# Kernel optimization log

Measured on AMD Instinct MI355X. Metric: run time of the kernel, lower is better.

Reference implementation:

```python
import jax, jax.numpy as jnp
import numpy as np

N_NODES = 50000
N_EDGES = 800000
NEG_SLOPE = 0.2


def _edge_softmax(scores, dst, n):
    # scores: [E, H]; softmax over edges grouped by destination node
    m = jax.ops.segment_max(scores, dst, num_segments=n)          # [N, H]
    ex = jnp.exp(scores - m[dst])                                 # [E, H]
    s = jax.ops.segment_sum(ex, dst, num_segments=n)              # [N, H]
    return ex / s[dst]


def _gat_layer(h, W, attn_l, attn_r, bias, src, dst, n, heads, out_d):
    feat = (h @ W).reshape(n, heads, out_d)                       # [N, H, D]
    el = jnp.sum(feat * attn_l, axis=-1)                          # [N, H]
    er = jnp.sum(feat * attn_r, axis=-1)                          # [N, H]
    e = jax.nn.leaky_relu(el[src] + er[dst], NEG_SLOPE)           # [E, H]
    alpha = _edge_softmax(e, dst, n)                              # [E, H]
    msg = feat[src] * alpha[:, :, None]                           # [E, H, D]
    rst = jax.ops.segment_sum(msg, dst, num_segments=n)           # [N, H, D]
    return rst + bias.reshape(1, heads, out_d)


def setup_inputs() -> dict:
    key = jax.random.key(0)
    ks = jax.random.split(key, 12)
    in_dim, hid, heads, out_dim = 128, 64, 4, 64
    sc = 0.1
    return {
        "emb": jax.random.normal(ks[0], (N_NODES, in_dim), jnp.float32),
        "src": jax.random.randint(ks[1], (N_EDGES,), 0, N_NODES, jnp.int32),
        "dst": jax.random.randint(ks[2], (N_EDGES,), 0, N_NODES, jnp.int32),
        "W1": jax.random.normal(ks[3], (in_dim, heads * hid), jnp.float32) * sc,
        "attn_l1": jax.random.normal(ks[4], (1, heads, hid), jnp.float32) * sc,
        "attn_r1": jax.random.normal(ks[5], (1, heads, hid), jnp.float32) * sc,
        "b1": jax.random.normal(ks[6], (heads * hid,), jnp.float32) * sc,
        "W2": jax.random.normal(ks[7], (heads * hid, out_dim), jnp.float32) * sc,
        "attn_l2": jax.random.normal(ks[8], (1, 1, out_dim), jnp.float32) * sc,
        "attn_r2": jax.random.normal(ks[9], (1, 1, out_dim), jnp.float32) * sc,
        "b2": jax.random.normal(ks[10], (out_dim,), jnp.float32) * sc,
    }


def reference(emb, src, dst, W1, attn_l1, attn_r1, b1, W2, attn_l2, attn_r2, b2):
    n = emb.shape[0]
    h = _gat_layer(emb, W1, attn_l1, attn_r1, b1, src, dst, n, 4, 64)   # [N,4,64]
    h = jax.nn.relu(h).reshape(n, 4 * 64)                                # [N,256]
    h = _gat_layer(h, W2, attn_l2, attn_r2, b2, src, dst, n, 1, 64)      # [N,1,64]
    return h.reshape(n, 64)
```

## Files before the change

kernel.cpp:

```cpp
#include <hip/hip_runtime.h>
#include <hip/hip_bf16.h>
#include <math.h>

#define DIV_UP(a,b) (((a)+(b)-1)/(b))

typedef __attribute__((ext_vector_type(8))) short short8v;
typedef __attribute__((ext_vector_type(4))) float f32x4;

__device__ __forceinline__ float bf_lo(unsigned u){ union{unsigned x; float f;} v; v.x = u << 16; return v.f; }
__device__ __forceinline__ float bf_hi(unsigned u){ union{unsigned x; float f;} v; v.x = u & 0xffff0000u; return v.f; }
__device__ __forceinline__ unsigned short f2bf(float f){
  union{float f; unsigned u;} v; v.f = f;
  unsigned r = v.u + 0x7fff + ((v.u >> 16) & 1);
  return (unsigned short)(r >> 16);
}
__device__ __forceinline__ unsigned packbf(float a, float b){
  return (unsigned)f2bf(a) | ((unsigned)f2bf(b) << 16);
}
__device__ __forceinline__ float lrelu(float x){ return x > 0.f ? x : 0.2f*x; }

__global__ void k_count_deg(const int* __restrict__ dst, int* __restrict__ deg, int E){
  int i = blockIdx.x*blockDim.x + threadIdx.x;
  if (i < E) atomicAdd(&deg[dst[i]], 1);
}

__global__ __launch_bounds__(256) void k_scan1(const int* __restrict__ deg,
                                               int* __restrict__ blocksum, int N){
  int b = blockIdx.x;
  int base = b*1024 + threadIdx.x*4;
  int s = 0;
  if (base + 3 < N){
    int4 v = *(const int4*)&deg[base];
    s = v.x + v.y + v.z + v.w;
  } else {
    for (int i = 0; i < 4; i++){ int idx = base + i; if (idx < N) s += deg[idx]; }
  }
  #pragma unroll
  for (int o = 32; o; o >>= 1) s += __shfl_down(s, o);
  __shared__ int ws[4];
  int wid = threadIdx.x >> 6, lane = threadIdx.x & 63;
  if (lane == 0) ws[wid] = s;
  __syncthreads();
  if (threadIdx.x == 0) blocksum[b] = ws[0] + ws[1] + ws[2] + ws[3];
}

__global__ void k_scan2(int* __restrict__ blocksum, int nb){
  int lane = threadIdx.x;
  int carry = 0;
  for (int base = 0; base < nb; base += 64){
    int idx = base + lane;
    int orig = (idx < nb) ? blocksum[idx] : 0;
    int v = orig;
    #pragma unroll
    for (int o = 1; o < 64; o <<= 1){ int t = __shfl_up(v, o); if (lane >= o) v += t; }
    if (idx < nb) blocksum[idx] = carry + v - orig;
    carry += __shfl(v, 63);
  }
}

__global__ __launch_bounds__(256) void k_scan3(const int* __restrict__ deg,
                                               const int* __restrict__ blockoff,
                                               int* __restrict__ row_start,
                                               int* __restrict__ cursor, int N){
  int b = blockIdx.x;
  int base = b*1024 + threadIdx.x*4;
  int v[4];
  #pragma unroll
  for (int i = 0; i < 4; i++){ int idx = base + i; v[i] = (idx < N) ? deg[idx] : 0; }
  int s = v[0] + v[1] + v[2] + v[3];
  int lane = threadIdx.x & 63, wid = threadIdx.x >> 6;
  int inc = s;
  #pragma unroll
  for (int o = 1; o < 64; o <<= 1){ int t = __shfl_up(inc, o); if (lane >= o) inc += t; }
  __shared__ int wsum[4];
  if (lane == 63) wsum[wid] = inc;
  __syncthreads();
  int woff = 0;
  #pragma unroll
  for (int i = 0; i < 4; i++) if (i < wid) woff += wsum[i];
  int run = blockoff[b] + woff + inc - s;
  #pragma unroll
  for (int i = 0; i < 4; i++){
    int idx = base + i;
    if (idx < N){ row_start[idx] = run; cursor[idx] = run; run += v[i]; }
  }
  if (base < N && base + 4 >= N) row_start[N] = run;
}

__global__ void k_fillw4(const int* __restrict__ dst, const int* __restrict__ src,
                         int* __restrict__ cursor, int* __restrict__ srcp,
                         int* __restrict__ dstp,
                         const float4* __restrict__ el4, const float4* __restrict__ er4,
                         float4* __restrict__ w4, int E){
  int i = blockIdx.x*blockDim.x + threadIdx.x;
  if (i < E){
    int d = dst[i], s = src[i];
    int p = atomicAdd(&cursor[d], 1);
    srcp[p] = s; dstp[p] = d;
    float4 l = el4[s], r = er4[d];
    float4 w;
    w.x = __expf(lrelu(l.x + r.x));
    w.y = __expf(lrelu(l.y + r.y));
    w.z = __expf(lrelu(l.z + r.z));
    w.w = __expf(lrelu(l.w + r.w));
    w4[p] = w;
  }
}

__global__ void k_edgew1(const int* __restrict__ srcp, const int* __restrict__ dstp,
                         const float* __restrict__ el, const float* __restrict__ er,
                         float* __restrict__ w1, int E){
  int i = blockIdx.x*blockDim.x + threadIdx.x;
  if (i < E) w1[i] = __expf(lrelu(el[srcp[i]] + er[dstp[i]]));
}

template<int K, int H, bool ABF>
__global__ __launch_bounds__(256) void k_gemm_mfma(const void* __restrict__ Av,
      const float* __restrict__ B, int ldb,
      unsigned short* __restrict__ Cbf,
      const float* __restrict__ al, const float* __restrict__ ar,
      float* __restrict__ el, float* __restrict__ er, int M){
  constexpr int KP = K + 8;
  __shared__ alignas(16) __hip_bfloat16 At[64][KP];
  __shared__ alignas(16) __hip_bfloat16 Bt[64][KP];
  __shared__ float elp[2][64], erp[2][64];
  const int tid = threadIdx.x;
  const int lane = tid & 63, w = tid >> 6;
  const int mw = w >> 1, nw = w & 1;
  const int m0 = blockIdx.x * 64, by = blockIdx.y, n0 = by * 64;

  if constexpr (!ABF){
    const float* A = (const float*)Av;
    #pragma unroll
    for (int i = 0; i < K/16; i++){
      int q = tid + i*256;
      int row = q / (K/4), c4 = q % (K/4);
      float4 a = make_float4(0.f,0.f,0.f,0.f);
      if (m0 + row < M) a = *(const float4*)&A[(size_t)(m0+row)*K + c4*4];
      *(uint2*)&At[row][c4*4] = make_uint2(packbf(a.x,a.y), packbf(a.z,a.w));
    }
  } else {
    const __hip_bfloat16* A = (const __hip_bfloat16*)Av;
    #pragma unroll
    for (int i = 0; i < K/32; i++){
      int q = tid + i*256;
      int row = q / (K/8), c8 = q % (K/8);
      uint4 u = make_uint4(0,0,0,0);
      if (m0 + row < M) u = *(const uint4*)&A[(size_t)(m0+row)*K + c8*8];
      *(uint4*)&At[row][c8*8] = u;
    }
  }
  #pragma unroll
  for (int i = 0; i < K/16; i++){
    int q = tid + i*256;
    int c = q & 63, k4 = q >> 6;
    float b0 = B[(size_t)(k4*4+0)*ldb + n0 + c];
    float b1 = B[(size_t)(k4*4+1)*ldb + n0 + c];
    float b2 = B[(size_t)(k4*4+2)*ldb + n0 + c];
    float b3 = B[(size_t)(k4*4+3)*ldb + n0 + c];
    *(uint2*)&Bt[c][k4*4] = make_uint2(packbf(b0,b1), packbf(b2,b3));
  }
  __syncthreads();

  f32x4 acc[2][2];
  #pragma unroll
  for (int i = 0; i < 2; i++)
    #pragma unroll
    for (int j = 0; j < 2; j++)
      #pragma unroll
      for (int r = 0; r < 4; r++) acc[i][j][r] = 0.f;

  const int rbase = mw*32, cbase = nw*32;
  const int fr = lane & 15, fg = lane >> 4;
  #pragma unroll
  for (int ks = 0; ks < K/32; ks++){
    short8v a0 = *(const short8v*)&At[rbase + fr     ][ks*32 + fg*8];
    short8v a1 = *(const short8v*)&At[rbase + 16 + fr][ks*32 + fg*8];
    short8v b0 = *(const short8v*)&Bt[cbase + fr     ][ks*32 + fg*8];
    short8v b1 = *(const short8v*)&Bt[cbase + 16 + fr][ks*32 + fg*8];
    acc[0][0] = __builtin_amdgcn_mfma_f32_16x16x32_bf16(a0, b0, acc[0][0], 0,0,0);
    acc[0][1] = __builtin_amdgcn_mfma_f32_16x16x32_bf16(a0, b1, acc[0][1], 0,0,0);
    acc[1][0] = __builtin_amdgcn_mfma_f32_16x16x32_bf16(a1, b0, acc[1][0], 0,0,0);
    acc[1][1] = __builtin_amdgcn_mfma_f32_16x16x32_bf16(a1, b1, acc[1][1], 0,0,0);
  }

  float alv[2], arv[2];
  #pragma unroll
  for (int nt = 0; nt < 2; nt++){
    int col = cbase + nt*16 + fr;
    alv[nt] = al[by*64 + col];
    arv[nt] = ar[by*64 + col];
  }
  #pragma unroll
  for (int mt = 0; mt < 2; mt++){
    #pragma unroll
    for (int r = 0; r < 4; r++){
      float pl = acc[mt][0][r]*alv[0] + acc[mt][1][r]*alv[1];
      float pr = acc[mt][0][r]*arv[0] + acc[mt][1][r]*arv[1];
      #pragma unroll
      for (int o = 1; o < 16; o <<= 1){ pl += __shfl_xor(pl, o); pr += __shfl_xor(pr, o); }
      if (fr == 0){
        int rl = rbase + mt*16 + fg*4 + r;
        elp[nw][rl] = pl; erp[nw][rl] = pr;
      }
    }
  }
  const int NN = H*64;
  #pragma unroll
  for (int mt = 0; mt < 2; mt++){
    #pragma unroll
    for (int r = 0; r < 4; r++){
      int row = m0 + rbase + mt*16 + fg*4 + r;
      if (row < M){
        #pragma unroll
        for (int nt = 0; nt < 2; nt++)
          Cbf[(size_t)row*NN + n0 + cbase + nt*16 + fr] = f2bf(acc[mt][nt][r]);
      }
    }
  }
  __syncthreads();
  if (tid < 64){
    int row = m0 + tid;
    if (row < M){
      el[(size_t)row*H + by] = elp[0][tid] + elp[1][tid];
      er[(size_t)row*H + by] = erp[0][tid] + erp[1][tid];
    }
  }
}

__global__ __launch_bounds__(256) void k_gath4(const char* __restrict__ featb,
      const float* __restrict__ w4, const int* __restrict__ row_start,
      const int* __restrict__ srcp, const float* __restrict__ bias,
      __hip_bfloat16* __restrict__ outb, int N, int nwaves){
  int wv = threadIdx.x >> 6, lane = threadIdx.x & 63;
  int g = lane >> 4, j = lane & 15, h = j >> 2;
  const char* fb = featb + (unsigned)(j << 5);

  int n = blockIdx.x*4 + wv;
  if (n >= N) return;
  int rs = row_start[n], re = row_start[n+1];

  while (true){
    int deg = re - rs;
    int nn = n + nwaves;
    int rs_n = 0, re_n = 0;
    if (nn < N){ rs_n = row_start[nn]; re_n = row_start[nn+1]; }

    float acc[16];
    #pragma unroll
    for (int k = 0; k < 16; k++) acc[k] = 0.f;
    float Sacc = 0.f;

    int i = 0;
    int full = deg & ~15;
    for (; i < full; i += 16){
      float wb[4]; uint4 u0[4], u1[4];
      #pragma unroll
      for (int k = 0; k < 4; k++){
        int e = rs + i + k*4 + g;
        int sb = srcp[e];
        wb[k] = w4[(size_t)e*4 + h];
        const char* p = fb + (size_t)sb*512u;
        u0[k] = *(const uint4*)p;
        u1[k] = *(const uint4*)(p + 16);
      }
      #pragma unroll
      for (int k = 0; k < 4; k++){
        float wk = wb[k];
        Sacc += wk;
        acc[0]  += bf_lo(u0[k].x)*wk; acc[1]  += bf_hi(u0[k].x)*wk;
        acc[2]  += bf_lo(u0[k].y)*wk; acc[3]  += bf_hi(u0[k].y)*wk;
        acc[4]  += bf_lo(u0[k].z)*wk; acc[5]  += bf_hi(u0[k].z)*wk;
        acc[6]  += bf_lo(u0[k].w)*wk; acc[7]  += bf_hi(u0[k].w)*wk;
        acc[8]  += bf_lo(u1[k].x)*wk; acc[9]  += bf_hi(u1[k].x)*wk;
        acc[10] += bf_lo(u1[k].y)*wk; acc[11] += bf_hi(u1[k].y)*wk;
        acc[12] += bf_lo(u1[k].z)*wk; acc[13] += bf_hi(u1[k].z)*wk;
        acc[14] += bf_lo(u1[k].w)*wk; acc[15] += bf_hi(u1[k].w)*wk;
      }
    }
    if (i < deg){
      float wb[4]; uint4 u0[4], u1[4];
      #pragma unroll
      for (int k = 0; k < 4; k++){
        int e = i + k*4 + g;
        wb[k] = 0.f;
        u0[k] = make_uint4(0,0,0,0); u1[k] = make_uint4(0,0,0,0);
        if (e < deg){
          int sb = srcp[rs + e];
          wb[k] = w4[(size_t)(rs + e)*4 + h];
          const char* p = fb + (size_t)sb*512u;
          u0[k] = *(const uint4*)p;
          u1[k] = *(const uint4*)(p + 16);
        }
      }
      #pragma unroll
      for (int k = 0; k < 4; k++){
        float wk = wb[k];
        Sacc += wk;
        acc[0]  += bf_lo(u0[k].x)*wk; acc[1]  += bf_hi(u0[k].x)*wk;
        acc[2]  += bf_lo(u0[k].y)*wk; acc[3]  += bf_hi(u0[k].y)*wk;
        acc[4]  += bf_lo(u0[k].z)*wk; acc[5]  += bf_hi(u0[k].z)*wk;
        acc[6]  += bf_lo(u0[k].w)*wk; acc[7]  += bf_hi(u0[k].w)*wk;
        acc[8]  += bf_lo(u1[k].x)*wk; acc[9]  += bf_hi(u1[k].x)*wk;
        acc[10] += bf_lo(u1[k].y)*wk; acc[11] += bf_hi(u1[k].y)*wk;
        acc[12] += bf_lo(u1[k].z)*wk; acc[13] += bf_hi(u1[k].z)*wk;
        acc[14] += bf_lo(u1[k].w)*wk; acc[15] += bf_hi(u1[k].w)*wk;
      }
    }

    #pragma unroll
    for (int k = 0; k < 16; k++){
      acc[k] += __shfl_xor(acc[k], 16);
      acc[k] += __shfl_xor(acc[k], 32);
    }
    Sacc += __shfl_xor(Sacc, 16);
    Sacc += __shfl_xor(Sacc, 32);
    if (g == 0){
      float inv = (deg > 0 && Sacc > 0.f) ? 1.f / Sacc : 0.f;
      float4 b0 = *(const float4*)&bias[j*16 + 0];
      float4 b1 = *(const float4*)&bias[j*16 + 4];
      float4 b2 = *(const float4*)&bias[j*16 + 8];
      float4 b3 = *(const float4*)&bias[j*16 + 12];
      float v[16];
      v[0]=acc[0]*inv+b0.x;  v[1]=acc[1]*inv+b0.y;  v[2]=acc[2]*inv+b0.z;  v[3]=acc[3]*inv+b0.w;
      v[4]=acc[4]*inv+b1.x;  v[5]=acc[5]*inv+b1.y;  v[6]=acc[6]*inv+b1.z;  v[7]=acc[7]*inv+b1.w;
      v[8]=acc[8]*inv+b2.x;  v[9]=acc[9]*inv+b2.y;  v[10]=acc[10]*inv+b2.z; v[11]=acc[11]*inv+b2.w;
      v[12]=acc[12]*inv+b3.x; v[13]=acc[13]*inv+b3.y; v[14]=acc[14]*inv+b3.z; v[15]=acc[15]*inv+b3.w;
      #pragma unroll
      for (int k = 0; k < 16; k++) v[k] = fmaxf(v[k], 0.f);
      uint4 o0, o1;
      o0.x = packbf(v[0], v[1]);   o0.y = packbf(v[2], v[3]);
      o0.z = packbf(v[4], v[5]);   o0.w = packbf(v[6], v[7]);
      o1.x = packbf(v[8], v[9]);   o1.y = packbf(v[10], v[11]);
      o1.z = packbf(v[12], v[13]); o1.w = packbf(v[14], v[15]);
      uint4* op = (uint4*)outb + (size_t)n*32 + (j << 1);
      op[0] = o0; op[1] = o1;
    }

    if (nn >= N) break;
    n = nn; rs = rs_n; re = re_n;
  }
}

__global__ __launch_bounds__(256) void k_gath1(const char* __restrict__ featb,
      const float* __restrict__ w1, const int* __restrict__ row_start,
      const int* __restrict__ srcp, const float* __restrict__ bias,
      float* __restrict__ out, int N, int nwaves){
  int wv = threadIdx.x >> 6, lane = threadIdx.x & 63;
  int g = lane >> 4, j = lane & 15;
  const char* fb = featb + (unsigned)(j << 3);

  int n = blockIdx.x*4 + wv;
  if (n >= N) return;
  int rs = row_start[n], re = row_start[n+1];

  while (true){
    int deg = re - rs;
    int nn = n + nwaves;
    int rs_n = 0, re_n = 0;
    if (nn < N){ rs_n = row_start[nn]; re_n = row_start[nn+1]; }

    float acc[4] = {0.f, 0.f, 0.f, 0.f};
    float Sacc = 0.f;

    int i = 0;
    int full = deg & ~15;
    for (; i < full; i += 16){
      float wb[4]; uint2 u[4];
      #pragma unroll
      for (int k = 0; k < 4; k++){
        int e = rs + i + k*4 + g;
        int sb = srcp[e];
        wb[k] = w1[e];
        u[k] = *(const uint2*)(fb + (size_t)sb*128u);
      }
      #pragma unroll
      for (int k = 0; k < 4; k++){
        float wk = wb[k];
        Sacc += wk;
        acc[0] += bf_lo(u[k].x)*wk; acc[1] += bf_hi(u[k].x)*wk;
        acc[2] += bf_lo(u[k].y)*wk; acc[3] += bf_hi(u[k].y)*wk;
      }
    }
    if (i < deg){
      float wb[4]; uint2 u[4];
      #pragma unroll
      for (int k = 0; k < 4; k++){
        int e = i + k*4 + g;
        wb[k] = 0.f;
        u[k] = make_uint2(0,0);
        if (e < deg){
          int sb = srcp[rs + e];
          wb[k] = w1[rs + e];
          u[k] = *(const uint2*)(fb + (size_t)sb*128u);
        }
      }
      #pragma unroll
      for (int k = 0; k < 4; k++){
        float wk = wb[k];
        Sacc += wk;
        acc[0] += bf_lo(u[k].x)*wk; acc[1] += bf_hi(u[k].x)*wk;
        acc[2] += bf_lo(u[k].y)*wk; acc[3] += bf_hi(u[k].y)*wk;
      }
    }

    #pragma unroll
    for (int k = 0; k < 4; k++){
      acc[k] += __shfl_xor(acc[k], 16);
      acc[k] += __shfl_xor(acc[k], 32);
    }
    Sacc += __shfl_xor(Sacc, 16);
    Sacc += __shfl_xor(Sacc, 32);
    if (g == 0){
      float inv = (deg > 0 && Sacc > 0.f) ? 1.f / Sacc : 0.f;
      float4 b = *(const float4*)&bias[j*4];
      float4 o;
      o.x = acc[0]*inv + b.x; o.y = acc[1]*inv + b.y;
      o.z = acc[2]*inv + b.z; o.w = acc[3]*inv + b.w;
      *(float4*)&out[(size_t)n*64 + j*4] = o;
    }

    if (nn >= N) break;
    n = nn; rs = rs_n; re = re_n;
  }
}

extern "C" void kernel_launch(void* const* d_in, const int* in_sizes, int n_in,
                              void* d_out, int out_size, void* d_ws, size_t ws_size,
                              hipStream_t stream) {
  const float* emb = (const float*)d_in[0];
  const int*   src = (const int*)d_in[1];
  const int*   dst = (const int*)d_in[2];
  const float* W1  = (const float*)d_in[3];
  const float* al1 = (const float*)d_in[4];
  const float* ar1 = (const float*)d_in[5];
  const float* b1  = (const float*)d_in[6];
  const float* W2  = (const float*)d_in[7];
  const float* al2 = (const float*)d_in[8];
  const float* ar2 = (const float*)d_in[9];
  const float* b2  = (const float*)d_in[10];
  float* out = (float*)d_out;

  const int N = in_sizes[0] / 128;
  const int E = in_sizes[1];

  char* p = (char*)d_ws;
  auto alloc = [&](size_t bytes) -> void* {
    void* r = (void*)p; p += (bytes + 255) & ~(size_t)255; return r;
  };
  __hip_bfloat16* feat1b = (__hip_bfloat16*)alloc((size_t)N*256*2);
  __hip_bfloat16* h1b    = (__hip_bfloat16*)alloc((size_t)N*256*2);
  __hip_bfloat16* feat2b = (__hip_bfloat16*)alloc((size_t)N*64*2);
  float* el1             = (float*)alloc((size_t)N*4*4);
  float* er1             = (float*)alloc((size_t)N*4*4);
  float* el2             = (float*)alloc((size_t)N*4);
  float* er2             = (float*)alloc((size_t)N*4);
  int*   deg             = (int*)alloc((size_t)N*4);
  int*   row_start       = (int*)alloc((size_t)(N+1)*4);
  int*   cursor          = (int*)alloc((size_t)N*4);
  int*   blocksum        = (int*)alloc((size_t)DIV_UP(N,1024)*4);
  int*   srcp            = (int*)alloc((size_t)E*4);
  int*   dstp            = (int*)alloc((size_t)E*4);
  float* w4              = (float*)alloc((size_t)E*16);
  float* w1              = w4;

  const int nb = DIV_UP(N, 1024);
  const int gblocks = min(DIV_UP(N, 4), 2048);
  const int nwaves  = gblocks * 4;

  hipMemsetAsync(deg, 0, (size_t)N*4, stream);
  k_count_deg<<<DIV_UP(E,256), 256, 0, stream>>>(dst, deg, E);
  k_scan1<<<nb, 256, 0, stream>>>(deg, blocksum, N);
  k_scan2<<<1, 64, 0, stream>>>(blocksum, nb);
  k_scan3<<<nb, 256, 0, stream>>>(deg, blocksum, row_start, cursor, N);

  k_gemm_mfma<128,4,false><<<dim3(DIV_UP(N,64), 4), 256, 0, stream>>>(
      emb, W1, 256, (unsigned short*)feat1b, al1, ar1, el1, er1, N);
  k_fillw4<<<DIV_UP(E,256), 256, 0, stream>>>(dst, src, cursor, srcp, dstp,
      (const float4*)el1, (const float4*)er1, (float4*)w4, E);
  k_gath4<<<gblocks, 256, 0, stream>>>((const char*)feat1b, w4, row_start,
                                       srcp, b1, h1b, N, nwaves);
  k_gemm_mfma<256,1,true><<<dim3(DIV_UP(N,64), 1), 256, 0, stream>>>(
      h1b, W2, 64, (unsigned short*)feat2b, al2, ar2, el2, er2, N);
  k_edgew1<<<DIV_UP(E,256), 256, 0, stream>>>(srcp, dstp, el2, er2, w1, E);
  k_gath1<<<gblocks, 256, 0, stream>>>((const char*)feat2b, w1, row_start,
                                       srcp, b2, out, N, nwaves);
}
```

Measured before the change: 237.7 us.

## Aggregate raw embeddings before the layer-1 projection, then apply W1 per head

Layer 1 now gathers bf16 input embeddings (128-wide) along edges and applies W1 afterwards, instead of gathering projected 256-wide features. Attention logits are computed directly from the embeddings using precomputed W1·attn vectors. The cost this targets is per-edge gather traffic: each edge now reads 256 B instead of 512 B. In exchange, each node stores a 4-head aggregate (512 bf16 values, larger than before) that the new per-head GEMM must re-read, and the gather does four times the FMAs per loaded element.

Result: slower. 264.0 us (+11.0%).

```diff
diff --git a/kernel.cpp b/kernel.cpp
--- a/kernel.cpp
+++ b/kernel.cpp
@@ -85,6 +85,46 @@
     if (idx < N){ row_start[idx] = run; cursor[idx] = run; run += v[i]; }
   }
   if (base < N && base + 4 >= N) row_start[N] = run;
+}
+
+__global__ __launch_bounds__(256) void k_prepvec(const float* __restrict__ W1,
+      const float* __restrict__ al, const float* __restrict__ ar,
+      float* __restrict__ W1al4, float* __restrict__ W1ar4){
+  int t = blockIdx.x*256 + threadIdx.x;
+  if (t >= 1024) return;
+  int k = t >> 3, idx = t & 7, h = idx >> 1, side = idx & 1;
+  const float* v = (side ? ar : al) + h*64;
+  const float* wrow = W1 + (size_t)k*256 + h*64;
+  float s = 0.f;
+  #pragma unroll 8
+  for (int d = 0; d < 64; d++) s += wrow[d]*v[d];
+  (side ? W1ar4 : W1al4)[k*4 + h] = s;
+}
+
+__global__ __launch_bounds__(256) void k_embcast(const float2* __restrict__ emb2,
+      const float4* __restrict__ W1al4, const float4* __restrict__ W1ar4,
+      unsigned* __restrict__ embb, float4* __restrict__ el4, float4* __restrict__ er4,
+      int N){
+  int wv = threadIdx.x >> 6, lane = threadIdx.x & 63;
+  int n = blockIdx.x*4 + wv;
+  if (n >= N) return;
+  float2 a = emb2[(size_t)n*64 + lane];
+  embb[(size_t)n*64 + lane] = packbf(a.x, a.y);
+  float4 wl0 = W1al4[2*lane], wl1 = W1al4[2*lane+1];
+  float4 wr0 = W1ar4[2*lane], wr1 = W1ar4[2*lane+1];
+  float4 pl, pr;
+  pl.x = a.x*wl0.x + a.y*wl1.x; pl.y = a.x*wl0.y + a.y*wl1.y;
+  pl.z = a.x*wl0.z + a.y*wl1.z; pl.w = a.x*wl0.w + a.y*wl1.w;
+  pr.x = a.x*wr0.x + a.y*wr1.x; pr.y = a.x*wr0.y + a.y*wr1.y;
+  pr.z = a.x*wr0.z + a.y*wr1.z; pr.w = a.x*wr0.w + a.y*wr1.w;
+  #pragma unroll
+  for (int o = 1; o < 64; o <<= 1){
+    pl.x += __shfl_xor(pl.x, o); pl.y += __shfl_xor(pl.y, o);
+    pl.z += __shfl_xor(pl.z, o); pl.w += __shfl_xor(pl.w, o);
+    pr.x += __shfl_xor(pr.x, o); pr.y += __shfl_xor(pr.y, o);
+    pr.z += __shfl_xor(pr.z, o); pr.w += __shfl_xor(pr.w, o);
+  }
+  if (lane == 0){ el4[n] = pl; er4[n] = pr; }
 }
 
 __global__ void k_fillw4(const int* __restrict__ dst, const int* __restrict__ src,
@@ -114,6 +154,186 @@
   if (i < E) w1[i] = __expf(lrelu(el[srcp[i]] + er[dstp[i]]));
 }
 
+__global__ __launch_bounds__(256) void k_gath4e(const char* __restrict__ embb,
+      const float4* __restrict__ w4, const int* __restrict__ row_start,
+      const int* __restrict__ srcp, uint4* __restrict__ aggb, int N, int nwaves){
+  int wv = threadIdx.x >> 6, lane = threadIdx.x & 63;
+  int g = lane >> 4, j = lane & 15;
+  const char* fb = embb + (unsigned)(j << 4);
+
+  int n = blockIdx.x*4 + wv;
+  if (n >= N) return;
+  int rs = row_start[n], re = row_start[n+1];
+
+  while (true){
+    int deg = re - rs;
+    int nn = n + nwaves;
+    int rs_n = 0, re_n = 0;
+    if (nn < N){ rs_n = row_start[nn]; re_n = row_start[nn+1]; }
+
+    float acc[4][8];
+    #pragma unroll
+    for (int h = 0; h < 4; h++)
+      #pragma unroll
+      for (int d = 0; d < 8; d++) acc[h][d] = 0.f;
+    float S0 = 0.f, S1 = 0.f, S2 = 0.f, S3 = 0.f;
+
+    int i = 0;
+    int full = deg & ~15;
+    for (; i < full; i += 16){
+      uint4 u[4]; float4 w[4];
+      #pragma unroll
+      for (int k = 0; k < 4; k++){
+        int e = rs + i + k*4 + g;
+        int sb = srcp[e];
+        w[k] = w4[e];
+        u[k] = *(const uint4*)(fb + (size_t)sb*256u);
+      }
+      #pragma unroll
+      for (int k = 0; k < 4; k++){
+        float4 wk = w[k];
+        S0 += wk.x; S1 += wk.y; S2 += wk.z; S3 += wk.w;
+        float x[8];
+        x[0]=bf_lo(u[k].x); x[1]=bf_hi(u[k].x); x[2]=bf_lo(u[k].y); x[3]=bf_hi(u[k].y);
+        x[4]=bf_lo(u[k].z); x[5]=bf_hi(u[k].z); x[6]=bf_lo(u[k].w); x[7]=bf_hi(u[k].w);
+        #pragma unroll
+        for (int d = 0; d < 8; d++){
+          acc[0][d] += x[d]*wk.x; acc[1][d] += x[d]*wk.y;
+          acc[2][d] += x[d]*wk.z; acc[3][d] += x[d]*wk.w;
+        }
+      }
+    }
+    if (i < deg){
+      uint4 u[4]; float4 w[4];
+      #pragma unroll
+      for (int k = 0; k < 4; k++){
+        int e = i + k*4 + g;
+        w[k] = make_float4(0.f,0.f,0.f,0.f);
+        u[k] = make_uint4(0,0,0,0);
+        if (e < deg){
+          int sb = srcp[rs + e];
+          w[k] = w4[rs + e];
+          u[k] = *(const uint4*)(fb + (size_t)sb*256u);
+        }
+      }
+      #pragma unroll
+      for (int k = 0; k < 4; k++){
+        float4 wk = w[k];
+        S0 += wk.x; S1 += wk.y; S2 += wk.z; S3 += wk.w;
+        float x[8];
+        x[0]=bf_lo(u[k].x); x[1]=bf_hi(u[k].x); x[2]=bf_lo(u[k].y); x[3]=bf_hi(u[k].y);
+        x[4]=bf_lo(u[k].z); x[5]=bf_hi(u[k].z); x[6]=bf_lo(u[k].w); x[7]=bf_hi(u[k].w);
+        #pragma unroll
+        for (int d = 0; d < 8; d++){
+          acc[0][d] += x[d]*wk.x; acc[1][d] += x[d]*wk.y;
+          acc[2][d] += x[d]*wk.z; acc[3][d] += x[d]*wk.w;
+        }
+      }
+    }
+
+    #pragma unroll
+    for (int h = 0; h < 4; h++)
+      #pragma unroll
+      for (int d = 0; d < 8; d++){
+        acc[h][d] += __shfl_xor(acc[h][d], 16);
+        acc[h][d] += __shfl_xor(acc[h][d], 32);
+      }
+    S0 += __shfl_xor(S0, 16); S0 += __shfl_xor(S0, 32);
+    S1 += __shfl_xor(S1, 16); S1 += __shfl_xor(S1, 32);
+    S2 += __shfl_xor(S2, 16); S2 += __shfl_xor(S2, 32);
+    S3 += __shfl_xor(S3, 16); S3 += __shfl_xor(S3, 32);
+
+    if (g == 0){
+      float Sv[4] = {S0, S1, S2, S3};
+      #pragma unroll
+      for (int h = 0; h < 4; h++){
+        float inv = (deg > 0 && Sv[h] > 0.f) ? 1.f/Sv[h] : 0.f;
+        uint4 o;
+        o.x = packbf(acc[h][0]*inv, acc[h][1]*inv);
+        o.y = packbf(acc[h][2]*inv, acc[h][3]*inv);
+        o.z = packbf(acc[h][4]*inv, acc[h][5]*inv);
+        o.w = packbf(acc[h][6]*inv, acc[h][7]*inv);
+        aggb[(size_t)n*64 + h*16 + j] = o;
+      }
+    }
+
+    if (nn >= N) break;
+    n = nn; rs = rs_n; re = re_n;
+  }
+}
+
+__global__ __launch_bounds__(256) void k_gemm_agg(const __hip_bfloat16* __restrict__ A,
+      const float* __restrict__ B,
+      const float* __restrict__ bias,
+      unsigned short* __restrict__ C,
+      int M){
+  __shared__ alignas(16) __hip_bfloat16 At[64][136];
+  __shared__ alignas(16) __hip_bfloat16 Bt[64][136];
+  const int tid = threadIdx.x;
+  const int lane = tid & 63, w = tid >> 6;
+  const int mw = w >> 1, nw = w & 1;
+  const int m0 = blockIdx.x * 64, by = blockIdx.y, n0 = by * 64;
+
+  #pragma unroll
+  for (int i = 0; i < 4; i++){
+    int q = tid + i*256;
+    int row = q >> 4, c8 = q & 15;
+    uint4 u = make_uint4(0,0,0,0);
+    if (m0 + row < M) u = *(const uint4*)&A[(size_t)(m0+row)*512 + by*128 + c8*8];
+    *(uint4*)&At[row][c8*8] = u;
+  }
+  #pragma unroll
+  for (int i = 0; i < 8; i++){
+    int q = tid + i*256;
+    int c = q & 63, k4 = q >> 6;
+    float b0 = B[(size_t)(k4*4+0)*256 + n0 + c];
+    float b1 = B[(size_t)(k4*4+1)*256 + n0 + c];
+    float b2 = B[(size_t)(k4*4+2)*256 + n0 + c];
+    float b3 = B[(size_t)(k4*4+3)*256 + n0 + c];
+    *(uint2*)&Bt[c][k4*4] = make_uint2(packbf(b0,b1), packbf(b2,b3));
+  }
+  __syncthreads();
+
+  f32x4 acc[2][2];
+  #pragma unroll
+  for (int i = 0; i < 2; i++)
+    #pragma unroll
+    for (int jj = 0; jj < 2; jj++)
+      #pragma unroll
+      for (int r = 0; r < 4; r++) acc[i][jj][r] = 0.f;
+
+  const int rbase = mw*32, cbase = nw*32;
+  const int fr = lane & 15, fg = lane >> 4;
+  #pragma unroll
+  for (int ks = 0; ks < 4; ks++){
+    short8v a0 = *(const short8v*)&At[rbase + fr     ][ks*32 + fg*8];
+    short8v a1 = *(const short8v*)&At[rbase + 16 + fr][ks*32 + fg*8];
+    short8v b0 = *(const short8v*)&Bt[cbase + fr     ][ks*32 + fg*8];
+    short8v b1 = *(const short8v*)&Bt[cbase + 16 + fr][ks*32 + fg*8];
+    acc[0][0] = __builtin_amdgcn_mfma_f32_16x16x32_bf16(a0, b0, acc[0][0], 0,0,0);
+    acc[0][1] = __builtin_amdgcn_mfma_f32_16x16x32_bf16(a0, b1, acc[0][1], 0,0,0);
+    acc[1][0] = __builtin_amdgcn_mfma_f32_16x16x32_bf16(a1, b0, acc[1][0], 0,0,0);
+    acc[1][1] = __builtin_amdgcn_mfma_f32_16x16x32_bf16(a1, b1, acc[1][1], 0,0,0);
+  }
+
+  #pragma unroll
+  for (int mt = 0; mt < 2; mt++){
+    #pragma unroll
+    for (int r = 0; r < 4; r++){
+      int row = m0 + rbase + mt*16 + fg*4 + r;
+      if (row < M){
+        #pragma unroll
+        for (int nt = 0; nt < 2; nt++){
+          int col = cbase + nt*16 + fr;
+          float v = acc[mt][nt][r] + bias[n0 + col];
+          v = fmaxf(v, 0.f);
+          C[(size_t)row*256 + n0 + col] = f2bf(v);
+        }
+      }
+    }
+  }
+}
+
 template<int K, int H, bool ABF>
 __global__ __launch_bounds__(256) void k_gemm_mfma(const void* __restrict__ Av,
       const float* __restrict__ B, int ldb,
@@ -225,120 +445,6 @@
       el[(size_t)row*H + by] = elp[0][tid] + elp[1][tid];
       er[(size_t)row*H + by] = erp[0][tid] + erp[1][tid];
     }
-  }
-}
-
-__global__ __launch_bounds__(256) void k_gath4(const char* __restrict__ featb,
-      const float* __restrict__ w4, const int* __restrict__ row_start,
-      const int* __restrict__ srcp, const float* __restrict__ bias,
-      __hip_bfloat16* __restrict__ outb, int N, int nwaves){
-  int wv = threadIdx.x >> 6, lane = threadIdx.x & 63;
-  int g = lane >> 4, j = lane & 15, h = j >> 2;
-  const char* fb = featb + (unsigned)(j << 5);
-
-  int n = blockIdx.x*4 + wv;
-  if (n >= N) return;
-  int rs = row_start[n], re = row_start[n+1];
-
-  while (true){
-    int deg = re - rs;
-    int nn = n + nwaves;
-    int rs_n = 0, re_n = 0;
-    if (nn < N){ rs_n = row_start[nn]; re_n = row_start[nn+1]; }
-
-    float acc[16];
-    #pragma unroll
-    for (int k = 0; k < 16; k++) acc[k] = 0.f;
-    float Sacc = 0.f;
-
-    int i = 0;
-    int full = deg & ~15;
-    for (; i < full; i += 16){
-      float wb[4]; uint4 u0[4], u1[4];
-      #pragma unroll
-      for (int k = 0; k < 4; k++){
-        int e = rs + i + k*4 + g;
-        int sb = srcp[e];
-        wb[k] = w4[(size_t)e*4 + h];
-        const char* p = fb + (size_t)sb*512u;
-        u0[k] = *(const uint4*)p;
-        u1[k] = *(const uint4*)(p + 16);
-      }
-      #pragma unroll
-      for (int k = 0; k < 4; k++){
-        float wk = wb[k];
-        Sacc += wk;
-        acc[0]  += bf_lo(u0[k].x)*wk; acc[1]  += bf_hi(u0[k].x)*wk;
-        acc[2]  += bf_lo(u0[k].y)*wk; acc[3]  += bf_hi(u0[k].y)*wk;
-        acc[4]  += bf_lo(u0[k].z)*wk; acc[5]  += bf_hi(u0[k].z)*wk;
-        acc[6]  += bf_lo(u0[k].w)*wk; acc[7]  += bf_hi(u0[k].w)*wk;
-        acc[8]  += bf_lo(u1[k].x)*wk; acc[9]  += bf_hi(u1[k].x)*wk;
-        acc[10] += bf_lo(u1[k].y)*wk; acc[11] += bf_hi(u1[k].y)*wk;
-        acc[12] += bf_lo(u1[k].z)*wk; acc[13] += bf_hi(u1[k].z)*wk;
-        acc[14] += bf_lo(u1[k].w)*wk; acc[15] += bf_hi(u1[k].w)*wk;
-      }
-    }
-    if (i < deg){
-      float wb[4]; uint4 u0[4], u1[4];
-      #pragma unroll
-      for (int k = 0; k < 4; k++){
-        int e = i + k*4 + g;
-        wb[k] = 0.f;
-        u0[k] = make_uint4(0,0,0,0); u1[k] = make_uint4(0,0,0,0);
-        if (e < deg){
-          int sb = srcp[rs + e];
-          wb[k] = w4[(size_t)(rs + e)*4 + h];
-          const char* p = fb + (size_t)sb*512u;
-          u0[k] = *(const uint4*)p;
-          u1[k] = *(const uint4*)(p + 16);
-        }
-      }
-      #pragma unroll
-      for (int k = 0; k < 4; k++){
-        float wk = wb[k];
-        Sacc += wk;
-        acc[0]  += bf_lo(u0[k].x)*wk; acc[1]  += bf_hi(u0[k].x)*wk;
-        acc[2]  += bf_lo(u0[k].y)*wk; acc[3]  += bf_hi(u0[k].y)*wk;
-        acc[4]  += bf_lo(u0[k].z)*wk; acc[5]  += bf_hi(u0[k].z)*wk;
-        acc[6]  += bf_lo(u0[k].w)*wk; acc[7]  += bf_hi(u0[k].w)*wk;
-        acc[8]  += bf_lo(u1[k].x)*wk; acc[9]  += bf_hi(u1[k].x)*wk;
-        acc[10] += bf_lo(u1[k].y)*wk; acc[11] += bf_hi(u1[k].y)*wk;
-        acc[12] += bf_lo(u1[k].z)*wk; acc[13] += bf_hi(u1[k].z)*wk;
-        acc[14] += bf_lo(u1[k].w)*wk; acc[15] += bf_hi(u1[k].w)*wk;
-      }
-    }
-
-    #pragma unroll
-    for (int k = 0; k < 16; k++){
-      acc[k] += __shfl_xor(acc[k], 16);
-      acc[k] += __shfl_xor(acc[k], 32);
-    }
-    Sacc += __shfl_xor(Sacc, 16);
-    Sacc += __shfl_xor(Sacc, 32);
-    if (g == 0){
-      float inv = (deg > 0 && Sacc > 0.f) ? 1.f / Sacc : 0.f;
-      float4 b0 = *(const float4*)&bias[j*16 + 0];
-      float4 b1 = *(const float4*)&bias[j*16 + 4];
-      float4 b2 = *(const float4*)&bias[j*16 + 8];
-      float4 b3 = *(const float4*)&bias[j*16 + 12];
-      float v[16];
-      v[0]=acc[0]*inv+b0.x;  v[1]=acc[1]*inv+b0.y;  v[2]=acc[2]*inv+b0.z;  v[3]=acc[3]*inv+b0.w;
-      v[4]=acc[4]*inv+b1.x;  v[5]=acc[5]*inv+b1.y;  v[6]=acc[6]*inv+b1.z;  v[7]=acc[7]*inv+b1.w;
-      v[8]=acc[8]*inv+b2.x;  v[9]=acc[9]*inv+b2.y;  v[10]=acc[10]*inv+b2.z; v[11]=acc[11]*inv+b2.w;
-      v[12]=acc[12]*inv+b3.x; v[13]=acc[13]*inv+b3.y; v[14]=acc[14]*inv+b3.z; v[15]=acc[15]*inv+b3.w;
-      #pragma unroll
-      for (int k = 0; k < 16; k++) v[k] = fmaxf(v[k], 0.f);
-      uint4 o0, o1;
-      o0.x = packbf(v[0], v[1]);   o0.y = packbf(v[2], v[3]);
-      o0.z = packbf(v[4], v[5]);   o0.w = packbf(v[6], v[7]);
-      o1.x = packbf(v[8], v[9]);   o1.y = packbf(v[10], v[11]);
-      o1.z = packbf(v[12], v[13]); o1.w = packbf(v[14], v[15]);
-      uint4* op = (uint4*)outb + (size_t)n*32 + (j << 1);
-      op[0] = o0; op[1] = o1;
-    }
-
-    if (nn >= N) break;
-    n = nn; rs = rs_n; re = re_n;
   }
 }
 
@@ -448,9 +554,12 @@
   auto alloc = [&](size_t bytes) -> void* {
     void* r = (void*)p; p += (bytes + 255) & ~(size_t)255; return r;
   };
-  __hip_bfloat16* feat1b = (__hip_bfloat16*)alloc((size_t)N*256*2);
+  __hip_bfloat16* embb   = (__hip_bfloat16*)alloc((size_t)N*128*2);
+  __hip_bfloat16* aggb   = (__hip_bfloat16*)alloc((size_t)N*512*2);
   __hip_bfloat16* h1b    = (__hip_bfloat16*)alloc((size_t)N*256*2);
   __hip_bfloat16* feat2b = (__hip_bfloat16*)alloc((size_t)N*64*2);
+  float* W1al4           = (float*)alloc(128*4*4);
+  float* W1ar4           = (float*)alloc(128*4*4);
   float* el1             = (float*)alloc((size_t)N*4*4);
   float* er1             = (float*)alloc((size_t)N*4*4);
   float* el2             = (float*)alloc((size_t)N*4);
@@ -474,12 +583,17 @@
   k_scan2<<<1, 64, 0, stream>>>(blocksum, nb);
   k_scan3<<<nb, 256, 0, stream>>>(deg, blocksum, row_start, cursor, N);
 
-  k_gemm_mfma<128,4,false><<<dim3(DIV_UP(N,64), 4), 256, 0, stream>>>(
-      emb, W1, 256, (unsigned short*)feat1b, al1, ar1, el1, er1, N);
+  k_prepvec<<<4, 256, 0, stream>>>(W1, al1, ar1, W1al4, W1ar4);
+  k_embcast<<<DIV_UP(N,4), 256, 0, stream>>>((const float2*)emb,
+      (const float4*)W1al4, (const float4*)W1ar4,
+      (unsigned*)embb, (float4*)el1, (float4*)er1, N);
   k_fillw4<<<DIV_UP(E,256), 256, 0, stream>>>(dst, src, cursor, srcp, dstp,
       (const float4*)el1, (const float4*)er1, (float4*)w4, E);
-  k_gath4<<<gblocks, 256, 0, stream>>>((const char*)feat1b, w4, row_start,
-                                       srcp, b1, h1b, N, nwaves);
+  k_gath4e<<<gblocks, 256, 0, stream>>>((const char*)embb, (const float4*)w4,
+      row_start, srcp, (uint4*)aggb, N, nwaves);
+  k_gemm_agg<<<dim3(DIV_UP(N,64), 4), 256, 0, stream>>>(aggb, W1, b1,
+      (unsigned short*)h1b, N);
+
   k_gemm_mfma<256,1,true><<<dim3(DIV_UP(N,64), 1), 256, 0, stream>>>(
       h1b, W2, 64, (unsigned short*)feat2b, al2, ar2, el2, er2, N);
   k_edgew1<<<DIV_UP(E,256), 256, 0, stream>>>(srcp, dstp, el2, er2, w1, E);
```

## Fuse edge weight computation into gather kernels and widen layer-1 GEMM tile

Applied to the files above, without the earlier changes.

Edge attention weights (exp of leaky-relu of el[src]+er[dst]) are now computed inside the aggregation kernels instead of being materialised per edge by the fill and edgew1 kernels. This drops the w4/w1/dstp arrays and one kernel launch, which removes the per-edge weight writes and reads. The cost is an extra gather of el per edge inside the aggregation loop, plus recomputing exp per head lane. The layer-1 GEMM is replaced by a 512-thread kernel that covers all 256 output columns per block, so the A tile is loaded once per block instead of once per head.

Measured after the change: 261.7 us. 1.1x slower.

```diff
diff --git a/kernel.cpp b/kernel.cpp
--- a/kernel.cpp
+++ b/kernel.cpp
@@ -87,31 +87,112 @@
   if (base < N && base + 4 >= N) row_start[N] = run;
 }
 
-__global__ void k_fillw4(const int* __restrict__ dst, const int* __restrict__ src,
-                         int* __restrict__ cursor, int* __restrict__ srcp,
-                         int* __restrict__ dstp,
-                         const float4* __restrict__ el4, const float4* __restrict__ er4,
-                         float4* __restrict__ w4, int E){
+__global__ void k_fill(const int* __restrict__ dst, const int* __restrict__ src,
+                       int* __restrict__ cursor, int* __restrict__ srcp, int E){
   int i = blockIdx.x*blockDim.x + threadIdx.x;
-  if (i < E){
-    int d = dst[i], s = src[i];
-    int p = atomicAdd(&cursor[d], 1);
-    srcp[p] = s; dstp[p] = d;
-    float4 l = el4[s], r = er4[d];
-    float4 w;
-    w.x = __expf(lrelu(l.x + r.x));
-    w.y = __expf(lrelu(l.y + r.y));
-    w.z = __expf(lrelu(l.z + r.z));
-    w.w = __expf(lrelu(l.w + r.w));
-    w4[p] = w;
-  }
-}
-
-__global__ void k_edgew1(const int* __restrict__ srcp, const int* __restrict__ dstp,
-                         const float* __restrict__ el, const float* __restrict__ er,
-                         float* __restrict__ w1, int E){
-  int i = blockIdx.x*blockDim.x + threadIdx.x;
-  if (i < E) w1[i] = __expf(lrelu(el[srcp[i]] + er[dstp[i]]));
+  if (i < E){ int p = atomicAdd(&cursor[dst[i]], 1); srcp[p] = src[i]; }
+}
+
+__global__ __launch_bounds__(512) void k_gemm1h4(const float* __restrict__ A,
+      const float* __restrict__ B,
+      unsigned short* __restrict__ Cbf,
+      const float* __restrict__ al, const float* __restrict__ ar,
+      float* __restrict__ el, float* __restrict__ er, int M){
+  __shared__ alignas(16) __hip_bfloat16 At[64][136];
+  __shared__ alignas(16) __hip_bfloat16 Bt[256][136];
+  __shared__ float elp[8][64], erp[8][64];
+  const int tid = threadIdx.x;
+  const int lane = tid & 63, w = tid >> 6;
+  const int m0 = blockIdx.x * 64;
+  const int fr = lane & 15, fg = lane >> 4;
+  const int cbase = w * 32;
+
+  #pragma unroll
+  for (int i = 0; i < 4; i++){
+    int q = tid + i*512;
+    int row = q >> 5, c4 = q & 31;
+    float4 a = make_float4(0.f,0.f,0.f,0.f);
+    if (m0 + row < M) a = *(const float4*)&A[(size_t)(m0+row)*128 + c4*4];
+    *(uint2*)&At[row][c4*4] = make_uint2(packbf(a.x,a.y), packbf(a.z,a.w));
+  }
+  #pragma unroll
+  for (int i = 0; i < 16; i++){
+    int q = tid + i*512;
+    int col = q & 255, k4 = q >> 8;
+    float b0 = B[(size_t)(k4*4+0)*256 + col];
+    float b1 = B[(size_t)(k4*4+1)*256 + col];
+    float b2 = B[(size_t)(k4*4+2)*256 + col];
+    float b3 = B[(size_t)(k4*4+3)*256 + col];
+    *(uint2*)&Bt[col][k4*4] = make_uint2(packbf(b0,b1), packbf(b2,b3));
+  }
+  __syncthreads();
+
+  f32x4 acc[4][2];
+  #pragma unroll
+  for (int mt = 0; mt < 4; mt++)
+    #pragma unroll
+    for (int nt = 0; nt < 2; nt++)
+      #pragma unroll
+      for (int r = 0; r < 4; r++) acc[mt][nt][r] = 0.f;
+
+  #pragma unroll
+  for (int ks = 0; ks < 4; ks++){
+    short8v a0 = *(const short8v*)&At[ 0 + fr][ks*32 + fg*8];
+    short8v a1 = *(const short8v*)&At[16 + fr][ks*32 + fg*8];
+    short8v a2 = *(const short8v*)&At[32 + fr][ks*32 + fg*8];
+    short8v a3 = *(const short8v*)&At[48 + fr][ks*32 + fg*8];
+    short8v b0 = *(const short8v*)&Bt[cbase      + fr][ks*32 + fg*8];
+    short8v b1 = *(const short8v*)&Bt[cbase + 16 + fr][ks*32 + fg*8];
+    acc[0][0] = __builtin_amdgcn_mfma_f32_16x16x32_bf16(a0, b0, acc[0][0], 0,0,0);
+    acc[0][1] = __builtin_amdgcn_mfma_f32_16x16x32_bf16(a0, b1, acc[0][1], 0,0,0);
+    acc[1][0] = __builtin_amdgcn_mfma_f32_16x16x32_bf16(a1, b0, acc[1][0], 0,0,0);
+    acc[1][1] = __builtin_amdgcn_mfma_f32_16x16x32_bf16(a1, b1, acc[1][1], 0,0,0);
+    acc[2][0] = __builtin_amdgcn_mfma_f32_16x16x32_bf16(a2, b0, acc[2][0], 0,0,0);
+    acc[2][1] = __builtin_amdgcn_mfma_f32_16x16x32_bf16(a2, b1, acc[2][1], 0,0,0);
+    acc[3][0] = __builtin_amdgcn_mfma_f32_16x16x32_bf16(a3, b0, acc[3][0], 0,0,0);
+    acc[3][1] = __builtin_amdgcn_mfma_f32_16x16x32_bf16(a3, b1, acc[3][1], 0,0,0);
+  }
+
+  float alv[2], arv[2];
+  #pragma unroll
+  for (int nt = 0; nt < 2; nt++){
+    int col = cbase + nt*16 + fr;
+    alv[nt] = al[col]; arv[nt] = ar[col];
+  }
+  #pragma unroll
+  for (int mt = 0; mt < 4; mt++){
+    #pragma unroll
+    for (int r = 0; r < 4; r++){
+      float pl = acc[mt][0][r]*alv[0] + acc[mt][1][r]*alv[1];
+      float pr = acc[mt][0][r]*arv[0] + acc[mt][1][r]*arv[1];
+      #pragma unroll
+      for (int o = 1; o < 16; o <<= 1){ pl += __shfl_xor(pl, o); pr += __shfl_xor(pr, o); }
+      if (fr == 0){
+        int rl = mt*16 + fg*4 + r;
+        elp[w][rl] = pl; erp[w][rl] = pr;
+      }
+    }
+  }
+  #pragma unroll
+  for (int mt = 0; mt < 4; mt++){
+    #pragma unroll
+    for (int r = 0; r < 4; r++){
+      int row = m0 + mt*16 + fg*4 + r;
+      if (row < M){
+        #pragma unroll
+        for (int nt = 0; nt < 2; nt++)
+          Cbf[(size_t)row*256 + cbase + nt*16 + fr] = f2bf(acc[mt][nt][r]);
+      }
+    }
+  }
+  __syncthreads();
+  if (tid < 256){
+    int row = tid & 63, h = tid >> 6;
+    if (m0 + row < M){
+      el[(size_t)(m0+row)*4 + h] = elp[2*h][row] + elp[2*h+1][row];
+      er[(size_t)(m0+row)*4 + h] = erp[2*h][row] + erp[2*h+1][row];
+    }
+  }
 }
 
 template<int K, int H, bool ABF>
@@ -228,10 +309,11 @@
   }
 }
 
-__global__ __launch_bounds__(256) void k_gath4(const char* __restrict__ featb,
-      const float* __restrict__ w4, const int* __restrict__ row_start,
-      const int* __restrict__ srcp, const float* __restrict__ bias,
-      __hip_bfloat16* __restrict__ outb, int N, int nwaves){
+__global__ __launch_bounds__(256) void k_gath4w(const char* __restrict__ featb,
+      const float4* __restrict__ el4, const float4* __restrict__ er4,
+      const int* __restrict__ row_start, const int* __restrict__ srcp,
+      const float* __restrict__ bias, __hip_bfloat16* __restrict__ outb,
+      int N, int nwaves){
   int wv = threadIdx.x >> 6, lane = threadIdx.x & 63;
   int g = lane >> 4, j = lane & 15, h = j >> 2;
   const char* fb = featb + (unsigned)(j << 5);
@@ -246,6 +328,9 @@
     int rs_n = 0, re_n = 0;
     if (nn < N){ rs_n = row_start[nn]; re_n = row_start[nn+1]; }
 
+    float4 ern = er4[n];
+    float ernh = (h==0) ? ern.x : (h==1) ? ern.y : (h==2) ? ern.z : ern.w;
+
     float acc[16];
     #pragma unroll
     for (int k = 0; k < 16; k++) acc[k] = 0.f;
@@ -254,40 +339,46 @@
     int i = 0;
     int full = deg & ~15;
     for (; i < full; i += 16){
-      float wb[4]; uint4 u0[4], u1[4];
+      float wk[4]; uint4 u0[4], u1[4];
       #pragma unroll
       for (int k = 0; k < 4; k++){
         int e = rs + i + k*4 + g;
         int sb = srcp[e];
-        wb[k] = w4[(size_t)e*4 + h];
+        float4 elv = el4[sb];
+        float xh = (h==0) ? elv.x : (h==1) ? elv.y : (h==2) ? elv.z : elv.w;
+        xh += ernh; xh = xh > 0.f ? xh : 0.2f*xh;
+        wk[k] = __expf(xh);
         const char* p = fb + (size_t)sb*512u;
         u0[k] = *(const uint4*)p;
         u1[k] = *(const uint4*)(p + 16);
       }
       #pragma unroll
       for (int k = 0; k < 4; k++){
-        float wk = wb[k];
-        Sacc += wk;
-        acc[0]  += bf_lo(u0[k].x)*wk; acc[1]  += bf_hi(u0[k].x)*wk;
-        acc[2]  += bf_lo(u0[k].y)*wk; acc[3]  += bf_hi(u0[k].y)*wk;
-        acc[4]  += bf_lo(u0[k].z)*wk; acc[5]  += bf_hi(u0[k].z)*wk;
-        acc[6]  += bf_lo(u0[k].w)*wk; acc[7]  += bf_hi(u0[k].w)*wk;
-        acc[8]  += bf_lo(u1[k].x)*wk; acc[9]  += bf_hi(u1[k].x)*wk;
-        acc[10] += bf_lo(u1[k].y)*wk; acc[11] += bf_hi(u1[k].y)*wk;
-        acc[12] += bf_lo(u1[k].z)*wk; acc[13] += bf_hi(u1[k].z)*wk;
-        acc[14] += bf_lo(u1[k].w)*wk; acc[15] += bf_hi(u1[k].w)*wk;
+        float w = wk[k];
+        Sacc += w;
+        acc[0]  += bf_lo(u0[k].x)*w; acc[1]  += bf_hi(u0[k].x)*w;
+        acc[2]  += bf_lo(u0[k].y)*w; acc[3]  += bf_hi(u0[k].y)*w;
+        acc[4]  += bf_lo(u0[k].z)*w; acc[5]  += bf_hi(u0[k].z)*w;
+        acc[6]  += bf_lo(u0[k].w)*w; acc[7]  += bf_hi(u0[k].w)*w;
+        acc[8]  += bf_lo(u1[k].x)*w; acc[9]  += bf_hi(u1[k].x)*w;
+        acc[10] += bf_lo(u1[k].y)*w; acc[11] += bf_hi(u1[k].y)*w;
+        acc[12] += bf_lo(u1[k].z)*w; acc[13] += bf_hi(u1[k].z)*w;
+        acc[14] += bf_lo(u1[k].w)*w; acc[15] += bf_hi(u1[k].w)*w;
       }
     }
     if (i < deg){
-      float wb[4]; uint4 u0[4], u1[4];
+      float wk[4]; uint4 u0[4], u1[4];
       #pragma unroll
       for (int k = 0; k < 4; k++){
         int e = i + k*4 + g;
-        wb[k] = 0.f;
+        wk[k] = 0.f;
         u0[k] = make_uint4(0,0,0,0); u1[k] = make_uint4(0,0,0,0);
         if (e < deg){
           int sb = srcp[rs + e];
-          wb[k] = w4[(size_t)(rs + e)*4 + h];
+          float4 elv = el4[sb];
+          float xh = (h==0) ? elv.x : (h==1) ? elv.y : (h==2) ? elv.z : elv.w;
+          xh += ernh; xh = xh > 0.f ? xh : 0.2f*xh;
+          wk[k] = __expf(xh);
           const char* p = fb + (size_t)sb*512u;
           u0[k] = *(const uint4*)p;
           u1[k] = *(const uint4*)(p + 16);
@@ -295,16 +386,16 @@
       }
       #pragma unroll
       for (int k = 0; k < 4; k++){
-        float wk = wb[k];
-        Sacc += wk;
-        acc[0]  += bf_lo(u0[k].x)*wk; acc[1]  += bf_hi(u0[k].x)*wk;
-        acc[2]  += bf_lo(u0[k].y)*wk; acc[3]  += bf_hi(u0[k].y)*wk;
-        acc[4]  += bf_lo(u0[k].z)*wk; acc[5]  += bf_hi(u0[k].z)*wk;
-        acc[6]  += bf_lo(u0[k].w)*wk; acc[7]  += bf_hi(u0[k].w)*wk;
-        acc[8]  += bf_lo(u1[k].x)*wk; acc[9]  += bf_hi(u1[k].x)*wk;
-        acc[10] += bf_lo(u1[k].y)*wk; acc[11] += bf_hi(u1[k].y)*wk;
-        acc[12] += bf_lo(u1[k].z)*wk; acc[13] += bf_hi(u1[k].z)*wk;
-        acc[14] += bf_lo(u1[k].w)*wk; acc[15] += bf_hi(u1[k].w)*wk;
+        float w = wk[k];
+        Sacc += w;
+        acc[0]  += bf_lo(u0[k].x)*w; acc[1]  += bf_hi(u0[k].x)*w;
+        acc[2]  += bf_lo(u0[k].y)*w; acc[3]  += bf_hi(u0[k].y)*w;
+        acc[4]  += bf_lo(u0[k].z)*w; acc[5]  += bf_hi(u0[k].z)*w;
+        acc[6]  += bf_lo(u0[k].w)*w; acc[7]  += bf_hi(u0[k].w)*w;
+        acc[8]  += bf_lo(u1[k].x)*w; acc[9]  += bf_hi(u1[k].x)*w;
+        acc[10] += bf_lo(u1[k].y)*w; acc[11] += bf_hi(u1[k].y)*w;
+        acc[12] += bf_lo(u1[k].z)*w; acc[13] += bf_hi(u1[k].z)*w;
+        acc[14] += bf_lo(u1[k].w)*w; acc[15] += bf_hi(u1[k].w)*w;
       }
     }
 
@@ -342,10 +433,10 @@
   }
 }
 
-__global__ __launch_bounds__(256) void k_gath1(const char* __restrict__ featb,
-      const float* __restrict__ w1, const int* __restrict__ row_start,
-      const int* __restrict__ srcp, const float* __restrict__ bias,
-      float* __restrict__ out, int N, int nwaves){
+__global__ __launch_bounds__(256) void k_gath1w(const char* __restrict__ featb,
+      const float* __restrict__ el, const float* __restrict__ er,
+      const int* __restrict__ row_start, const int* __restrict__ srcp,
+      const float* __restrict__ bias, float* __restrict__ out, int N, int nwaves){
   int wv = threadIdx.x >> 6, lane = threadIdx.x & 63;
   int g = lane >> 4, j = lane & 15;
   const char* fb = featb + (unsigned)(j << 3);
@@ -360,47 +451,52 @@
     int rs_n = 0, re_n = 0;
     if (nn < N){ rs_n = row_start[nn]; re_n = row_start[nn+1]; }
 
+    float ern = er[n];
     float acc[4] = {0.f, 0.f, 0.f, 0.f};
     float Sacc = 0.f;
 
     int i = 0;
     int full = deg & ~15;
     for (; i < full; i += 16){
-      float wb[4]; uint2 u[4];
+      float wk[4]; uint2 u[4];
       #pragma unroll
       for (int k = 0; k < 4; k++){
         int e = rs + i + k*4 + g;
         int sb = srcp[e];
-        wb[k] = w1[e];
+        float x = el[sb] + ern;
+        x = x > 0.f ? x : 0.2f*x;
+        wk[k] = __expf(x);
         u[k] = *(const uint2*)(fb + (size_t)sb*128u);
       }
       #pragma unroll
       for (int k = 0; k < 4; k++){
-        float wk = wb[k];
-        Sacc += wk;
-        acc[0] += bf_lo(u[k].x)*wk; acc[1] += bf_hi(u[k].x)*wk;
-        acc[2] += bf_lo(u[k].y)*wk; acc[3] += bf_hi(u[k].y)*wk;
+        float w = wk[k];
+        Sacc += w;
+        acc[0] += bf_lo(u[k].x)*w; acc[1] += bf_hi(u[k].x)*w;
+        acc[2] += bf_lo(u[k].y)*w; acc[3] += bf_hi(u[k].y)*w;
       }
     }
     if (i < deg){
-      float wb[4]; uint2 u[4];
+      float wk[4]; uint2 u[4];
       #pragma unroll
       for (int k = 0; k < 4; k++){
         int e = i + k*4 + g;
-        wb[k] = 0.f;
+        wk[k] = 0.f;
         u[k] = make_uint2(0,0);
         if (e < deg){
           int sb = srcp[rs + e];
-          wb[k] = w1[rs + e];
+          float x = el[sb] + ern;
+          x = x > 0.f ? x : 0.2f*x;
+          wk[k] = __expf(x);
           u[k] = *(const uint2*)(fb + (size_t)sb*128u);
         }
       }
       #pragma unroll
       for (int k = 0; k < 4; k++){
-        float wk = wb[k];
-        Sacc += wk;
-        acc[0] += bf_lo(u[k].x)*wk; acc[1] += bf_hi(u[k].x)*wk;
-        acc[2] += bf_lo(u[k].y)*wk; acc[3] += bf_hi(u[k].y)*wk;
+        float w = wk[k];
+        Sacc += w;
+        acc[0] += bf_lo(u[k].x)*w; acc[1] += bf_hi(u[k].x)*w;
+        acc[2] += bf_lo(u[k].y)*w; acc[3] += bf_hi(u[k].y)*w;
       }
     }
 
@@ -460,9 +556,6 @@
   int*   cursor          = (int*)alloc((size_t)N*4);
   int*   blocksum        = (int*)alloc((size_t)DIV_UP(N,1024)*4);
   int*   srcp            = (int*)alloc((size_t)E*4);
-  int*   dstp            = (int*)alloc((size_t)E*4);
-  float* w4              = (float*)alloc((size_t)E*16);
-  float* w1              = w4;
 
   const int nb = DIV_UP(N, 1024);
   const int gblocks = min(DIV_UP(N, 4), 2048);
@@ -473,16 +566,14 @@
   k_scan1<<<nb, 256, 0, stream>>>(deg, blocksum, N);
   k_scan2<<<1, 64, 0, stream>>>(blocksum, nb);
   k_scan3<<<nb, 256, 0, stream>>>(deg, blocksum, row_start, cursor, N);
-
-  k_gemm_mfma<128,4,false><<<dim3(DIV_UP(N,64), 4), 256, 0, stream>>>(
-      emb, W1, 256, (unsigned short*)feat1b, al1, ar1, el1, er1, N);
-  k_fillw4<<<DIV_UP(E,256), 256, 0, stream>>>(dst, src, cursor, srcp, dstp,
-      (const float4*)el1, (const float4*)er1, (float4*)w4, E);
-  k_gath4<<<gblocks, 256, 0, stream>>>((const char*)feat1b, w4, row_start,
-                                       srcp, b1, h1b, N, nwaves);
+  k_fill<<<DIV_UP(E,256), 256, 0, stream>>>(dst, src, cursor, srcp, E);
+
+  k_gemm1h4<<<DIV_UP(N,64), 512, 0, stream>>>(emb, W1, (unsigned short*)feat1b,
+                                              al1, ar1, el1, er1, N);
+  k_gath4w<<<gblocks, 256, 0, stream>>>((const char*)feat1b, (const float4*)el1,
+      (const float4*)er1, row_start, srcp, b1, h1b, N, nwaves);
   k_gemm_mfma<256,1,true><<<dim3(DIV_UP(N,64), 1), 256, 0, stream>>>(
       h1b, W2, 64, (unsigned short*)feat2b, al2, ar2, el2, er2, N);
-  k_edgew1<<<DIV_UP(E,256), 256, 0, stream>>>(srcp, dstp, el2, er2, w1, E);
-  k_gath1<<<gblocks, 256, 0, stream>>>((const char*)feat2b, w1, row_start,
-                                       srcp, b2, out, N, nwaves);
-}
+  k_gath1w<<<gblocks, 256, 0, stream>>>((const char*)feat2b, el2, er2,
+      row_start, srcp, b2, out, N, nwaves);
+}
```
